# Optimization experiments

Hardware: AMD Instinct MI355X
Metric: run time of the kernel (lower is better)

## Reference

```python
import jax, jax.numpy as jnp
import numpy as np

B, H, W, C = 2, 128, 128, 96
L = H * W
NUM_HEADS = 6
D_STATE = 16
DT_RANK = 6  # ceil(96/16)
D_CONV = 4
MLP_HIDDEN = 4 * C


def _layernorm(x, g, b, eps=1e-5):
    m = x.mean(-1, keepdims=True)
    v = x.var(-1, keepdims=True)
    return (x - m) * jax.lax.rsqrt(v + eps) * g + b


def _dwconv2d(x, w, b):
    # x: [B,C,H,W], w: [C,1,3,3] depthwise, padding=1 (torch 'same' for k=3)
    y = jax.lax.conv_general_dilated(x, w, (1, 1), [(1, 1), (1, 1)],
                                     dimension_numbers=('NCHW', 'OIHW', 'NCHW'),
                                     feature_group_count=x.shape[1])
    return y + b[None, :, None, None]


def _dwconv1d(x, w):
    # x: [B,C,L], w: [C,1,4]; torch padding='same' for even k=4 pads (1,2); bias is None (conv_bias//2 == 0)
    return jax.lax.conv_general_dilated(x, w, (1,), [(1, 2)],
                                        dimension_numbers=('NCH', 'OIH', 'NCH'),
                                        feature_group_count=x.shape[1])


def _rope(x):
    # x: [b, H, W, c]; 2D axial rotary embedding, k_max = c//4 per axis
    b, h, w, c = x.shape
    k_max = c // 4
    theta = 1.0 / (10000.0 ** (jnp.arange(k_max, dtype=jnp.float32) / k_max))
    ang_h = jnp.broadcast_to(jnp.arange(h, dtype=jnp.float32)[:, None, None] * theta, (h, w, k_max))
    ang_w = jnp.broadcast_to(jnp.arange(w, dtype=jnp.float32)[None, :, None] * theta, (h, w, k_max))
    angles = jnp.concatenate([ang_h, ang_w], -1)  # [h,w,c//2]
    cos, sin = jnp.cos(angles), jnp.sin(angles)
    xr, xi = x[..., 0::2], x[..., 1::2]  # consecutive pairs -> complex
    out_r = xr * cos - xi * sin
    out_i = xr * sin + xi * cos
    return jnp.stack([out_r, out_i], -1).reshape(x.shape)


def _linear_attention(x, qk_w, qk_b, lepe_w, lepe_b):
    # x: [b, n, c]
    b, n, c = x.shape
    hd = c // NUM_HEADS
    qk = x @ qk_w + qk_b  # [b,n,2c]
    q = jax.nn.elu(qk[..., :c]) + 1.0
    k = jax.nn.elu(qk[..., c:]) + 1.0
    v = x
    q_r = _rope(q.reshape(b, H, W, c)).reshape(b, n, NUM_HEADS, hd).transpose(0, 2, 1, 3)
    k_r = _rope(k.reshape(b, H, W, c)).reshape(b, n, NUM_HEADS, hd).transpose(0, 2, 1, 3)
    qh = q.reshape(b, n, NUM_HEADS, hd).transpose(0, 2, 1, 3)
    kh = k.reshape(b, n, NUM_HEADS, hd).transpose(0, 2, 1, 3)
    vh = v.reshape(b, n, NUM_HEADS, hd).transpose(0, 2, 1, 3)
    kmean = kh.mean(axis=2, keepdims=True)  # [b,h,1,hd]
    zden = 1.0 / (jnp.einsum('bhnd,bhmd->bhnm', qh, kmean) + 1e-6)  # [b,h,n,1]
    scale = n ** (-0.5)
    kv = jnp.einsum('bhnd,bhne->bhde', k_r * scale, vh * scale)  # [b,h,hd,hd]
    out = jnp.einsum('bhnd,bhde->bhne', q_r, kv) * zden
    out = out.transpose(0, 2, 1, 3).reshape(b, n, c)
    v2d = v.reshape(b, H, W, c).transpose(0, 3, 1, 2)
    lepe = _dwconv2d(v2d, lepe_w, lepe_b).transpose(0, 2, 3, 1).reshape(b, n, c)
    return out + lepe


def _selective_scan(u, delta, A, Bm, Cm, Dv):
    # u, delta: [b,d,l]; A: [d,n]; Bm, Cm: [b,n,l]; Dv: [d]
    dA = jnp.exp(jnp.einsum('bdl,dn->lbdn', delta, A))
    dBu = jnp.einsum('bdl,bnl,bdl->lbdn', delta, Bm, u)
    Ct = jnp.moveaxis(Cm, -1, 0)  # [l,b,n]

    def step(hcar, inp):
        dA_t, dBu_t, C_t = inp
        hcar = dA_t * hcar + dBu_t  # [b,d,n]
        y_t = jnp.einsum('bdn,bn->bd', hcar, C_t)
        return hcar, y_t

    h0 = jnp.zeros(dA.shape[1:], dtype=u.dtype)
    _, ys = jax.lax.scan(step, h0, (dA, dBu, Ct))  # ys: [l,b,d]
    y = jnp.moveaxis(ys, 0, -1)  # [b,d,l]
    return y + Dv[None, :, None] * u


def setup_inputs() -> dict:
    key = jax.random.key(0)
    ks = iter(jax.random.split(key, 40))

    def rn(shape, s=0.02):
        return jax.random.normal(next(ks), shape, jnp.float32) * s

    dt = jnp.exp(jax.random.uniform(next(ks), (C,), jnp.float32)
                 * (np.log(0.1) - np.log(0.001)) + np.log(0.001))
    dt_proj_b = dt + jnp.log(-jnp.expm1(-dt))
    return {
        'hidden_states': jax.random.normal(next(ks), (B, L, C), jnp.float32),
        'norm_in_g': jnp.ones((C,), jnp.float32),
        'norm_in_b': jnp.zeros((C,), jnp.float32),
        'in_proj_w': rn((C, 3 * C)),
        'dw_w': rn((C, 1, 3, 3)),
        'dw_b': rn((C,)),
        'qk_w': rn((C, 2 * C)),
        'qk_b': rn((2 * C,)),
        'lepe_w': rn((C, 1, 3, 3)),
        'lepe_b': rn((C,)),
        'conv_x_w': rn((C, 1, D_CONV)),
        'conv_z_w': rn((C, 1, D_CONV)),
        'x_proj_w': rn((C, DT_RANK + 2 * D_STATE)),
        'dt_proj_w': rn((DT_RANK, C), DT_RANK ** -0.5),
        'dt_proj_b': dt_proj_b,
        'A_log': jnp.log(jnp.broadcast_to(jnp.arange(1, D_STATE + 1, dtype=jnp.float32), (C, D_STATE)) + 0.0),
        'D': jnp.ones((C,), jnp.float32),
        'out_proj_w': rn((2 * C, C)),
        'proj_out_w': rn((C, C)),
        'proj_out_b': rn((C,)),
        'out_w': rn((2 * C, C)),
        'out_b': rn((C,)),
        'norm_mlp_g': jnp.ones((C,), jnp.float32),
        'norm_mlp_b': jnp.zeros((C,), jnp.float32),
        'fc1_w': rn((C, MLP_HIDDEN)),
        'fc1_b': rn((MLP_HIDDEN,)),
        'fc2_w': rn((MLP_HIDDEN, C)),
        'fc2_b': rn((C,)),
    }


def reference(hidden_states, norm_in_g, norm_in_b, in_proj_w, dw_w, dw_b, qk_w, qk_b,
              lepe_w, lepe_b, conv_x_w, conv_z_w, x_proj_w, dt_proj_w, dt_proj_b,
              A_log, D, out_proj_w, proj_out_w, proj_out_b, out_w, out_b,
              norm_mlp_g, norm_mlp_b, fc1_w, fc1_b, fc2_w, fc2_b):
    b, l, c = hidden_states.shape
    shortcut = hidden_states
    hs = _layernorm(hidden_states, norm_in_g, norm_in_b)
    xzw = jnp.transpose(hs @ in_proj_w, (0, 2, 1))  # [b,3c,l]
    x, z, w_ = jnp.split(xzw, 3, axis=1)  # each [b,c,l]
    # linear-attention branch
    lin_x = jax.nn.silu(_dwconv2d(w_.reshape(b, c, H, W), dw_w, dw_b))
    lin_x = jnp.transpose(lin_x, (0, 2, 3, 1)).reshape(b, l, c)
    lin_x = _linear_attention(lin_x, qk_w, qk_b, lepe_w, lepe_b)
    # selective-scan branch
    A = -jnp.exp(A_log)
    x = jax.nn.silu(_dwconv1d(x, conv_x_w))
    z = jax.nn.silu(_dwconv1d(z, conv_z_w))
    x_dbl = jnp.einsum('bdl,de->ble', x, x_proj_w)
    dt = x_dbl[..., :DT_RANK]
    Bm = jnp.transpose(x_dbl[..., DT_RANK:DT_RANK + D_STATE], (0, 2, 1))
    Cm = jnp.transpose(x_dbl[..., DT_RANK + D_STATE:], (0, 2, 1))
    delta = jax.nn.softplus(jnp.einsum('blr,rd->bdl', dt, dt_proj_w) + dt_proj_b[None, :, None])
    y = _selective_scan(x, delta, A, Bm, Cm, D)
    y = jnp.concatenate([y, z], axis=1)  # [b,2c,l]
    out1 = jnp.transpose(y, (0, 2, 1)) @ out_proj_w  # [b,l,c]
    z_t = jnp.transpose(z, (0, 2, 1))
    out2 = (lin_x * z_t) @ proj_out_w + proj_out_b
    out = jnp.concatenate([out1, out2], -1) @ out_w + out_b
    out = shortcut + out
    h2 = _layernorm(out, norm_mlp_g, norm_mlp_b)
    h2 = jax.nn.gelu(h2 @ fc1_w + fc1_b, approximate=False)
    return out + (h2 @ fc2_w + fc2_b)
```

## Files before the change

kernel.cpp:

```cpp
#include <hip/hip_runtime.h>
#include <hip/hip_bf16.h>
#include <math.h>

#define B_ 2
#define H_ 128
#define W_ 128
#define C_ 96
#define L_ (H_*W_)
#define BL_ (B_*L_)
#define NH_ 6
#define NPROJ_ 38
#define MLPH_ 384
#define NCH_ 256
#define CHL_ (L_/NCH_)

typedef __attribute__((ext_vector_type(8))) short bf16x8;
typedef __attribute__((ext_vector_type(4))) float f32x4;

#define MFMA16(a,b,c) __builtin_amdgcn_mfma_f32_16x16x32_bf16(a,b,c,0,0,0)

#define WOFF1 0
#define WOFF2 54
#define WOFF3 90
#define WOFF4 126
#define WOFF5 144
#define WOFF6 180
#define WOFF7 252
#define WOFF8 324
#define WFRAGS 333

__device__ __forceinline__ float siluf(float x){ return x / (1.f + __expf(-x)); }
__device__ __forceinline__ unsigned short f2bf(float x){
    __hip_bfloat16 h = __float2bfloat16(x);
    return *reinterpret_cast<unsigned short*>(&h);
}
__device__ __forceinline__ unsigned pack2(float a, float b){
    return (unsigned)f2bf(a) | ((unsigned)f2bf(b) << 16);
}
__device__ __forceinline__ float bf2f(unsigned short u){
    return __uint_as_float((unsigned)u << 16);
}

__global__ __launch_bounds__(64) void k_setup(const float* __restrict__ w1,
    const float* __restrict__ w2, const float* __restrict__ w3,
    const float* __restrict__ w4, const float* __restrict__ w5,
    const float* __restrict__ w6, const float* __restrict__ w7,
    const float* __restrict__ dww, const float* __restrict__ lw,
    const float* __restrict__ xpw, const float* __restrict__ cxw,
    const float* __restrict__ czw,
    unsigned short* __restrict__ dst, float2* __restrict__ ctab,
    float* __restrict__ wt9, float* __restrict__ lw9, float* __restrict__ kvacc,
    float* __restrict__ wxT, float* __restrict__ wzT)
{
    int m = blockIdx.y;
    int l = threadIdx.x;
    if (m < 7){
        const float* srcs[7] = {w1,w2,w3,w4,w5,w6,w7};
        const int Ks[7]   = {96,96,192,96,192,96,384};
        const int Ns[7]   = {288,192,96,96,96,384,96};
        const int offs[7] = {WOFF1,WOFF2,WOFF3,WOFF4,WOFF5,WOFF6,WOFF7};
        int f = blockIdx.x;
        int nnt = Ns[m] >> 4, nkf = Ks[m] >> 5;
        if (f >= nnt*nkf) return;
        int kf = f / nnt, nt = f - kf*nnt;
        const float* s = srcs[m];
        unsigned short* d = dst + ((size_t)(offs[m] + f)*64 + l)*8;
        int krow = kf*32 + (l>>4)*8;
        int col  = nt*16 + (l&15);
        #pragma unroll
        for (int j=0;j<8;j++) d[j] = f2bf(s[(size_t)(krow+j)*Ns[m] + col]);
    } else {
        int x = blockIdx.x;
        if (x == 0){
            for (int i=l; i<128*24; i+=64){
                int pos = i/24, p = i%24;
                float th = powf(10000.f, -(float)p/24.f);
                float sn, cs; sincosf((float)pos*th, &sn, &cs);
                ctab[i] = make_float2(cs, sn);
            }
        } else if (x == 1){
            for (int i=l; i<3264; i+=64) kvacc[i] = 0.f;
        } else if (x == 2){
            for (int i=l; i<864; i+=64){
                int c = i/9, tap = i%9;
                wt9[tap*96 + c] = dww[i];
                lw9[tap*96 + c] = lw[i];
            }
        } else if (x == 3){
            for (int f=0; f<9; f++){
                int kf=f/3, nt=f%3;
                unsigned short* d = dst + ((size_t)(WOFF8 + f)*64 + l)*8;
                int krow = kf*32 + (l>>4)*8;
                int col  = nt*16 + (l&15);
                #pragma unroll
                for (int j=0;j<8;j++){
                    float v = (col < NPROJ_) ? xpw[(size_t)(krow+j)*NPROJ_ + col] : 0.f;
                    d[j] = f2bf(v);
                }
            }
        } else if (x == 4){
            for (int i=l; i<384; i+=64){
                int j = i/96, c = i%96;
                wxT[i] = cxw[c*4 + j];
                wzT[i] = czw[c*4 + j];
            }
        }
    }
}

__global__ __launch_bounds__(256) void k_ln_inproj_m(const float* __restrict__ hs,
    const float* __restrict__ gg, const float* __restrict__ bb,
    const unsigned short* __restrict__ wbf,
    float* __restrict__ xx, float* __restrict__ zz, float* __restrict__ ww)
{
    __shared__ unsigned short A[64*128];
    int t = threadIdx.x;
    size_t row0 = (size_t)blockIdx.x * 64;
    {
        int r = t >> 2, q = t & 3;
        const float* src = hs + (row0 + r)*C_ + q*24;
        float v[24];
        float s=0.f, s2=0.f;
        #pragma unroll
        for (int i=0;i<24;i++){ float x=src[i]; v[i]=x; s+=x; s2+=x*x; }
        s += __shfl_xor(s,1); s2 += __shfl_xor(s2,1);
        s += __shfl_xor(s,2); s2 += __shfl_xor(s2,2);
        float mn = s*(1.f/C_);
        float rs = rsqrtf(s2*(1.f/C_) - mn*mn + 1e-5f);
        int base = r*128, sw = (r&7)<<3;
        #pragma unroll
        for (int i=0;i<24;i+=2){
            int c = q*24 + i;
            float a0 = (v[i]  -mn)*rs*gg[c]   + bb[c];
            float a1 = (v[i+1]-mn)*rs*gg[c+1] + bb[c+1];
            *(unsigned*)&A[base + (c ^ sw)] = pack2(a0,a1);
        }
    }
    __syncthreads();
    int w = t>>6, l = t&63, lr = l&15, lh = l>>4;
    int arow = w*16 + lr;
    int abase = arow*128, asw = (arow&7)<<3;
    bf16x8 af[3];
    #pragma unroll
    for (int kf=0;kf<3;kf++)
        af[kf] = *(const bf16x8*)&A[abase + ((kf*32 + lh*8) ^ asw)];
    #pragma unroll 2
    for (int nt=0; nt<18; nt++){
        f32x4 acc = {0.f,0.f,0.f,0.f};
        #pragma unroll
        for (int kf=0;kf<3;kf++){
            bf16x8 bf_ = *(const bf16x8*)(wbf + ((size_t)((WOFF1 + kf*18 + nt)*64 + l))*8);
            acc = MFMA16(af[kf], bf_, acc);
        }
        float* base_;
        if (nt < 6) base_ = xx; else if (nt < 12) base_ = zz; else base_ = ww;
        int col = (nt%6)*16 + lr;
        float* dst = base_ + (row0 + w*16 + lh*4)*C_ + col;
        #pragma unroll
        for (int j=0;j<4;j++) dst[(size_t)j*C_] = acc[j];
    }
}

__global__ __launch_bounds__(256) void k_dwconv2d(const float* __restrict__ wwb,
    const float* __restrict__ wt9, const float* __restrict__ dwb,
    float* __restrict__ out)
{
    int gid = blockIdx.x*256 + threadIdx.x;
    int row = gid/24, c4 = gid%24; int c = c4*4;
    int b = row >> 14;
    int ll = row & (L_-1);
    int h = ll >> 7, wq = ll & 127;
    float4 acc = {0.f,0.f,0.f,0.f};
    #pragma unroll
    for (int kh=0; kh<3; kh++){
        int hh = h + kh - 1;
        if ((unsigned)hh < 128u){
            int base_row = (b<<14) + (hh<<7);
            #pragma unroll
            for (int kw=0; kw<3; kw++){
                int wp = wq + kw - 1;
                if ((unsigned)wp < 128u){
                    float4 v = *(const float4*)&wwb[(size_t)(base_row + wp)*C_ + c];
                    float4 wt = *(const float4*)&wt9[(kh*3+kw)*96 + c];
                    acc.x += v.x*wt.x; acc.y += v.y*wt.y;
                    acc.z += v.z*wt.z; acc.w += v.w*wt.w;
                }
            }
        }
    }
    float4 bv = *(const float4*)&dwb[c];
    float4 o;
    o.x = siluf(acc.x+bv.x); o.y = siluf(acc.y+bv.y);
    o.z = siluf(acc.z+bv.z); o.w = siluf(acc.w+bv.w);
    *(float4*)&out[(size_t)row*C_ + c] = o;
}

__global__ __launch_bounds__(256) void k_conv1d_xdbl(const float* __restrict__ xxb,
    const float* __restrict__ zzb, const float* __restrict__ wxT,
    const float* __restrict__ wzT, const unsigned short* __restrict__ wbf,
    const float* __restrict__ dtw, const float* __restrict__ dtb,
    float* __restrict__ xs, float* __restrict__ zs,
    float* __restrict__ delta, float* __restrict__ BC)
{
    __shared__ unsigned short A[64*128];
    __shared__ float XD[64][8];
    __shared__ float dtws[6][96];
    int t = threadIdx.x;
    size_t row0 = (size_t)blockIdx.x * 64;
    int b = (int)(row0 >> 14);
    int l0 = (int)(row0 & 16383);
    for (int i=t; i<576; i+=256) dtws[i/96][i%96] = dtw[i];
    for (int p=t; p<64*24; p+=256){
        int r = p/24, cq = p - r*24, c = cq*4;
        int l = l0 + r;
        float ax0=0.f,ax1=0.f,ax2=0.f,ax3=0.f;
        float az0=0.f,az1=0.f,az2=0.f,az3=0.f;
        #pragma unroll
        for (int j=0;j<4;j++){
            int lq = l - 1 + j;
            if ((unsigned)lq < (unsigned)L_){
                size_t off = ((size_t)(b<<14) + lq)*C_ + c;
                float4 xv = *(const float4*)&xxb[off];
                float4 zv = *(const float4*)&zzb[off];
                float4 wx4 = *(const float4*)&wxT[j*96 + c];
                float4 wz4 = *(const float4*)&wzT[j*96 + c];
                ax0 += xv.x*wx4.x; ax1 += xv.y*wx4.y; ax2 += xv.z*wx4.z; ax3 += xv.w*wx4.w;
                az0 += zv.x*wz4.x; az1 += zv.y*wz4.y; az2 += zv.z*wz4.z; az3 += zv.w*wz4.w;
            }
        }
        ax0=siluf(ax0); ax1=siluf(ax1); ax2=siluf(ax2); ax3=siluf(ax3);
        az0=siluf(az0); az1=siluf(az1); az2=siluf(az2); az3=siluf(az3);
        float4 xo={ax0,ax1,ax2,ax3}, zo={az0,az1,az2,az3};
        *(float4*)&xs[(row0+r)*C_ + c] = xo;
        *(float4*)&zs[(row0+r)*C_ + c] = zo;
        int sw = (r&7)<<3;
        uint2 pk = { pack2(ax0,ax1), pack2(ax2,ax3) };
        *(uint2*)&A[r*128 + (c ^ sw)] = pk;
    }
    __syncthreads();
    int w=t>>6, l=t&63, lr=l&15, lh=l>>4;
    int arow = w*16+lr, asw=(arow&7)<<3;
    bf16x8 af[3];
    #pragma unroll
    for (int kf=0;kf<3;kf++)
        af[kf] = *(const bf16x8*)&A[arow*128 + ((kf*32 + lh*8) ^ asw)];
    #pragma unroll
    for (int nt=0; nt<3; nt++){
        f32x4 acc={0.f,0.f,0.f,0.f};
        #pragma unroll
        for (int kf=0;kf<3;kf++){
            bf16x8 bfr=*(const bf16x8*)(wbf + ((size_t)((WOFF8 + kf*3 + nt)*64 + l))*8);
            acc = MFMA16(af[kf], bfr, acc);
        }
        int col = nt*16 + lr;
        #pragma unroll
        for (int j=0;j<4;j++){
            int row = w*16 + lh*4 + j;
            if (col < 6) XD[row][col] = acc[j];
            else if (col < NPROJ_) BC[(row0+row)*32 + (col-6)] = acc[j];
        }
    }
    __syncthreads();
    {
        int r = t>>2, q = t&3;
        float xd0=XD[r][0], xd1=XD[r][1], xd2=XD[r][2];
        float xd3=XD[r][3], xd4=XD[r][4], xd5=XD[r][5];
        #pragma unroll
        for (int g=0; g<6; g++){
            int c = q*24 + g*4;
            float4 acc = *(const float4*)&dtb[c];
            float4 w0 = *(const float4*)&dtws[0][c];
            float4 w1 = *(const float4*)&dtws[1][c];
            float4 w2 = *(const float4*)&dtws[2][c];
            float4 w3 = *(const float4*)&dtws[3][c];
            float4 w4 = *(const float4*)&dtws[4][c];
            float4 w5 = *(const float4*)&dtws[5][c];
            acc.x += xd0*w0.x + xd1*w1.x + xd2*w2.x + xd3*w3.x + xd4*w4.x + xd5*w5.x;
            acc.y += xd0*w0.y + xd1*w1.y + xd2*w2.y + xd3*w3.y + xd4*w4.y + xd5*w5.y;
            acc.z += xd0*w0.z + xd1*w1.z + xd2*w2.z + xd3*w3.z + xd4*w4.z + xd5*w5.z;
            acc.w += xd0*w0.w + xd1*w1.w + xd2*w2.w + xd3*w3.w + xd4*w4.w + xd5*w5.w;
            float4 dl;
            dl.x = (acc.x>20.f)? acc.x : __logf(1.f+__expf(acc.x));
            dl.y = (acc.y>20.f)? acc.y : __logf(1.f+__expf(acc.y));
            dl.z = (acc.z>20.f)? acc.z : __logf(1.f+__expf(acc.z));
            dl.w = (acc.w>20.f)? acc.w : __logf(1.f+__expf(acc.w));
            *(float4*)&delta[(row0+r)*C_ + c] = dl;
        }
    }
}

__global__ __launch_bounds__(256) void k_qk_kv(const float* __restrict__ lin,
    const unsigned short* __restrict__ wbf, const float* __restrict__ qkb,
    const float2* __restrict__ ctab, float* __restrict__ qo,
    float* __restrict__ kvacc)
{
    __shared__ unsigned short A[64*128];
    __shared__ float KR[64*105];
    __shared__ float kmsum[96];
    int t = threadIdx.x;
    size_t row0 = (size_t)blockIdx.x * 64;
    int b = (int)(row0 >> 14);
    int l0 = (int)(row0 & 16383);
    for (int p = t; p < 64*48; p += 256){
        int r = p/48, c = (p - r*48)*2;
        float2 xy = *(const float2*)&lin[(row0 + r)*C_ + c];
        *(unsigned*)&A[r*128 + (c ^ ((r&7)<<3))] = pack2(xy.x, xy.y);
    }
    if (t < 96) kmsum[t] = 0.f;
    __syncthreads();
    int w=t>>6, l=t&63, lr=l&15, lh=l>>4;
    int arow = w*16+lr; int asw=(arow&7)<<3;
    bf16x8 af[3];
    #pragma unroll
    for (int kf=0;kf<3;kf++)
        af[kf] = *(const bf16x8*)&A[arow*128 + ((kf*32 + lh*8) ^ asw)];
    #pragma unroll 2
    for (int nt=0; nt<12; nt++){
        f32x4 acc={0.f,0.f,0.f,0.f};
        #pragma unroll
        for (int kf=0;kf<3;kf++){
            bf16x8 bfr=*(const bf16x8*)(wbf + ((size_t)((WOFF2 + kf*12 + nt)*64 + l))*8);
            acc = MFMA16(af[kf], bfr, acc);
        }
        int colg = nt*16 + lr;
        float bias = qkb[colg];
        float vv[4];
        #pragma unroll
        for (int j=0;j<4;j++){
            float v = acc[j] + bias;
            vv[j] = (v>0.f)? v+1.f : __expf(v);
        }
        if (nt < 6){
            float* dp = qo + (row0 + w*16 + lh*4)*C_ + colg;
            #pragma unroll
            for (int j=0;j<4;j++) dp[(size_t)j*C_] = vv[j];
        } else {
            int ck = colg - 96;
            atomicAdd(&kmsum[ck], vv[0]+vv[1]+vv[2]+vv[3]);
            float pv[4];
            #pragma unroll
            for (int j=0;j<4;j++) pv[j] = __shfl_xor(vv[j], 1);
            int p = ck >> 1;
            #pragma unroll
            for (int j=0;j<4;j++){
                int rl = l0 + w*16 + lh*4 + j;
                int hp = rl>>7, wp = rl&127;
                float2 cssn = (p<24)? ctab[hp*24+p] : ctab[wp*24+(p-24)];
                float kr = (ck&1)? (pv[j]*cssn.y + vv[j]*cssn.x)
                                 : (vv[j]*cssn.x - pv[j]*cssn.y);
                KR[(w*16+lh*4+j)*105 + ck] = kr;
            }
        }
    }
    __syncthreads();
    if (w < 2){
        #pragma unroll
        for (int hh=0; hh<3; hh++){
            int h = w*3 + hh;
            f32x4 acc = {0.f,0.f,0.f,0.f};
            #pragma unroll
            for (int kk=0; kk<2; kk++){
                union { bf16x8 v; unsigned short u[8]; } afu, bfu;
                #pragma unroll
                for (int j=0;j<8;j++){
                    int rr = kk*32 + lh*8 + j;
                    afu.u[j] = f2bf(KR[rr*105 + h*16 + lr]);
                    bfu.u[j] = A[rr*128 + ((h*16+lr) ^ ((rr&7)<<3))];
                }
                acc = MFMA16(afu.v, bfu.v, acc);
            }
            #pragma unroll
            for (int i=0;i<4;i++)
                atomicAdd(&kvacc[b*1536 + h*256 + (lh*4+i)*16 + lr], acc[i]);
        }
    }
    if (t < 96) atomicAdd(&kvacc[3072 + b*96 + t], kmsum[t]);
}

__global__ __launch_bounds__(384) void k_attnout(const float* __restrict__ qbuf,
    const float* __restrict__ vbuf, const float* __restrict__ kvacc,
    const float2* __restrict__ ctab, const float* __restrict__ lw9,
    const float* __restrict__ lb, float* __restrict__ aout)
{
    __shared__ float kvs[1536];
    __shared__ float kms[96];
    int t = threadIdx.x;
    size_t row0 = (size_t)blockIdx.x * 16;
    int b = (int)(row0 >> 14);
    const float invL = 1.f/16384.f;
    for (int i=t; i<1536; i+=384) kvs[i] = kvacc[b*1536+i]*invL;
    if (t < 96) kms[t] = kvacc[3072+b*96+t]*invL;
    __syncthreads();
    int r = t/24, c4 = t%24;
    int c = c4*4;
    int lrow = (int)(row0 & 16383) + r;
    int hp = lrow>>7, wp = lrow&127;
    size_t row = row0 + r;
    float4 q4 = *(const float4*)&qbuf[row*C_ + c];
    int p0 = c>>1, p1 = p0+1;
    float2 cs0 = (p0<24)? ctab[hp*24+p0] : ctab[wp*24+(p0-24)];
    float2 cs1 = (p1<24)? ctab[hp*24+p1] : ctab[wp*24+(p1-24)];
    float4 qr;
    qr.x = q4.x*cs0.x - q4.y*cs0.y;
    qr.y = q4.x*cs0.y + q4.y*cs0.x;
    qr.z = q4.z*cs1.x - q4.w*cs1.y;
    qr.w = q4.z*cs1.y + q4.w*cs1.x;
    int h = c4>>2, j = c4&3;
    int dbase = j*4;
    float zp = q4.x*kms[h*16+dbase]   + q4.y*kms[h*16+dbase+1]
             + q4.z*kms[h*16+dbase+2] + q4.w*kms[h*16+dbase+3];
    zp += __shfl_xor(zp,1);
    zp += __shfl_xor(zp,2);
    float zd = 1.f/(zp + 1e-6f);
    float4 o = {0.f,0.f,0.f,0.f};
    #pragma unroll
    for (int g=0; g<4; g++){
        float4 qg;
        if (g==0) qg = qr;
        else {
            qg.x=__shfl_xor(qr.x,g); qg.y=__shfl_xor(qr.y,g);
            qg.z=__shfl_xor(qr.z,g); qg.w=__shfl_xor(qr.w,g);
        }
        int db = ((j^g)<<2);
        const float* kp = &kvs[h*256 + db*16 + j*4];
        #pragma unroll
        for (int i=0;i<4;i++){
            float qi = (i==0)?qg.x:(i==1)?qg.y:(i==2)?qg.z:qg.w;
            float4 kv4 = *(const float4*)&kp[i*16];
            o.x += qi*kv4.x; o.y += qi*kv4.y;
            o.z += qi*kv4.z; o.w += qi*kv4.w;
        }
    }
    float4 acc = *(const float4*)&lb[c];
    #pragma unroll
    for (int kh=0; kh<3; kh++){
        int hh = hp + kh - 1;
        if ((unsigned)hh < 128u){
            int base_row = (b<<14) + (hh<<7);
            #pragma unroll
            for (int kw=0; kw<3; kw++){
                int wq = wp + kw - 1;
                if ((unsigned)wq < 128u){
                    float4 v = *(const float4*)&vbuf[(size_t)(base_row + wq)*C_ + c];
                    float4 wt = *(const float4*)&lw9[(kh*3+kw)*96 + c];
                    acc.x += v.x*wt.x; acc.y += v.y*wt.y;
                    acc.z += v.z*wt.z; acc.w += v.w*wt.w;
                }
            }
        }
    }
    float4 res;
    res.x = o.x*zd + acc.x; res.y = o.y*zd + acc.y;
    res.z = o.z*zd + acc.z; res.w = o.w*zd + acc.w;
    *(float4*)&aout[row*C_ + c] = res;
}

__global__ __launch_bounds__(384) void k_scan1(const float* __restrict__ delta,
    const float* __restrict__ xs, const float* __restrict__ BC,
    const float* __restrict__ A_log, float* __restrict__ Ap, float* __restrict__ Be)
{
    int t = threadIdx.x; int nq = t&3, c = t>>2;
    int blk = blockIdx.x; int b = blk>>8, ch = blk&255;
    float4 a4 = *(const float4*)&A_log[c*16 + nq*4];
    float a0=-__expf(a4.x), a1=-__expf(a4.y), a2=-__expf(a4.z), a3=-__expf(a4.w);
    float ap0=1.f,ap1=1.f,ap2=1.f,ap3=1.f;
    float be0=0.f,be1=0.f,be2=0.f,be3=0.f;
    size_t base = ((size_t)b<<14) + ch*CHL_;
    for (int i=0;i<CHL_;i++){
        size_t row = base + i;
        float dl = delta[row*C_+c];
        float u  = xs[row*C_+c];
        float du = dl*u;
        float4 bc = *(const float4*)&BC[row*32 + nq*4];
        float e0=__expf(dl*a0), e1=__expf(dl*a1), e2=__expf(dl*a2), e3=__expf(dl*a3);
        ap0*=e0; be0=be0*e0+du*bc.x;
        ap1*=e1; be1=be1*e1+du*bc.y;
        ap2*=e2; be2=be2*e2+du*bc.z;
        ap3*=e3; be3=be3*e3+du*bc.w;
    }
    size_t o = (size_t)blk*1536 + c*16 + nq*4;
    float4 apv={ap0,ap1,ap2,ap3}, bev={be0,be1,be2,be3};
    *(float4*)&Ap[o] = apv;
    *(float4*)&Be[o] = bev;
}

__global__ __launch_bounds__(384) void k_scan2a(const float* __restrict__ Ap,
    const float* __restrict__ Be, float* __restrict__ GA, float* __restrict__ GB)
{
    int t = threadIdx.x; int blk = blockIdx.x;
    int b = blk>>4, g = blk&15;
    int idx = (t>>2)*16 + (t&3)*4;
    float4 A = {1.f,1.f,1.f,1.f}, Bv = {0.f,0.f,0.f,0.f};
    for (int j=0;j<16;j++){
        size_t o = ((size_t)(b*256 + g*16 + j))*1536 + idx;
        float4 a = *(const float4*)&Ap[o];
        float4 bb = *(const float4*)&Be[o];
        Bv.x=a.x*Bv.x+bb.x; Bv.y=a.y*Bv.y+bb.y; Bv.z=a.z*Bv.z+bb.z; Bv.w=a.w*Bv.w+bb.w;
        A.x*=a.x; A.y*=a.y; A.z*=a.z; A.w*=a.w;
    }
    size_t o = (size_t)blk*1536 + idx;
    *(float4*)&GA[o] = A;
    *(float4*)&GB[o] = Bv;
}

__global__ __launch_bounds__(256) void k_scan2b(const float* __restrict__ GA,
    const float* __restrict__ GB, float* __restrict__ Gin)
{
    int t = blockIdx.x*256 + threadIdx.x;
    int b = t/1536, m = t%1536;
    float h = 0.f;
    for (int g=0; g<16; g++){
        size_t o = ((size_t)(b*16+g))*1536 + m;
        Gin[o] = h;
        h = GA[o]*h + GB[o];
    }
}

__global__ __launch_bounds__(384) void k_scan2c(const float* __restrict__ Ap,
    const float* __restrict__ Be, const float* __restrict__ Gin,
    float* __restrict__ Hin)
{
    int t = threadIdx.x; int blk = blockIdx.x;
    int b = blk>>4, g = blk&15;
    int idx = (t>>2)*16 + (t&3)*4;
    float4 h = *(const float4*)&Gin[(size_t)blk*1536 + idx];
    for (int j=0;j<16;j++){
        size_t o = ((size_t)(b*256 + g*16 + j))*1536 + idx;
        *(float4*)&Hin[o] = h;
        float4 a = *(const float4*)&Ap[o];
        float4 bb = *(const float4*)&Be[o];
        h.x=a.x*h.x+bb.x; h.y=a.y*h.y+bb.y; h.z=a.z*h.z+bb.z; h.w=a.w*h.w+bb.w;
    }
}

__global__ __launch_bounds__(384) void k_scan3(const float* __restrict__ delta,
    const float* __restrict__ xs, const float* __restrict__ BC,
    const float* __restrict__ A_log, const float* __restrict__ Dv,
    const float* __restrict__ Hin, float* __restrict__ y)
{
    int t = threadIdx.x; int nq = t&3, c = t>>2;
    int blk = blockIdx.x; int b = blk>>8, ch = blk&255;
    float4 a4 = *(const float4*)&A_log[c*16 + nq*4];
    float a0=-__expf(a4.x), a1=-__expf(a4.y), a2=-__expf(a4.z), a3=-__expf(a4.w);
    float4 h = *(const float4*)&Hin[(size_t)blk*1536 + c*16 + nq*4];
    float Dc = Dv[c];
    size_t base = ((size_t)b<<14) + ch*CHL_;
    for (int i=0;i<CHL_;i++){
        size_t row = base + i;
        float dl = delta[row*C_+c];
        float u  = xs[row*C_+c];
        float du = dl*u;
        float4 bcB = *(const float4*)&BC[row*32 + nq*4];
        float4 bcC = *(const float4*)&BC[row*32 + 16 + nq*4];
        float e0=__expf(dl*a0), e1=__expf(dl*a1), e2=__expf(dl*a2), e3=__expf(dl*a3);
        h.x=h.x*e0+du*bcB.x; h.y=h.y*e1+du*bcB.y;
        h.z=h.z*e2+du*bcB.z; h.w=h.w*e3+du*bcB.w;
        float yv = h.x*bcC.x + h.y*bcC.y + h.z*bcC.z + h.w*bcC.w;
        yv += __shfl_xor(yv,1);
        yv += __shfl_xor(yv,2);
        if (nq == 0) y[row*C_+c] = yv + Dc*u;
    }
}

__global__ __launch_bounds__(256) void k_combine_m(const float* __restrict__ y,
    const float* __restrict__ zs, const float* __restrict__ aout,
    const unsigned short* __restrict__ wbf, const float* __restrict__ pob,
    const float* __restrict__ outb, const float* __restrict__ hs,
    float* __restrict__ outr)
{
    __shared__ unsigned short Y[64*192];
    __shared__ unsigned short AZ[64*128];
    __shared__ unsigned short C2[64*192];
    int t=threadIdx.x;
    size_t row0=(size_t)blockIdx.x*64;
    for (int p=t;p<64*48;p+=256){
        int r=p/48, c=(p-r*48)*2;
        size_t g=(row0+r)*C_+c;
        float2 yv=*(const float2*)&y[g];
        float2 zv=*(const float2*)&zs[g];
        float2 av=*(const float2*)&aout[g];
        int sw=(r&7)<<3;
        *(unsigned*)&Y[r*192 + (c^sw)] = pack2(yv.x,yv.y);
        *(unsigned*)&Y[r*192 + ((96+c)^sw)] = pack2(zv.x,zv.y);
        *(unsigned*)&AZ[r*128 + (c^sw)] = pack2(av.x*zv.x, av.y*zv.y);
    }
    __syncthreads();
    int w=t>>6,l=t&63,lr=l&15,lh=l>>4;
    int arow=w*16+lr; int asw=(arow&7)<<3;
    bf16x8 af1[6], af2[3];
    #pragma unroll
    for (int kf=0;kf<6;kf++) af1[kf]=*(const bf16x8*)&Y[arow*192 + ((kf*32+lh*8)^asw)];
    #pragma unroll
    for (int kf=0;kf<3;kf++) af2[kf]=*(const bf16x8*)&AZ[arow*128 + ((kf*32+lh*8)^asw)];
    #pragma unroll 2
    for (int nt=0;nt<6;nt++){
        f32x4 a1={0.f,0.f,0.f,0.f}, a2={0.f,0.f,0.f,0.f};
        #pragma unroll
        for (int kf=0;kf<6;kf++){
            bf16x8 b=*(const bf16x8*)(wbf+((size_t)((WOFF3+kf*6+nt)*64+l))*8);
            a1=MFMA16(af1[kf],b,a1);
        }
        #pragma unroll
        for (int kf=0;kf<3;kf++){
            bf16x8 b=*(const bf16x8*)(wbf+((size_t)((WOFF4+kf*6+nt)*64+l))*8);
            a2=MFMA16(af2[kf],b,a2);
        }
        int col=nt*16+lr;
        float pb=pob[col];
        #pragma unroll
        for (int j=0;j<4;j++){
            int row=w*16+lh*4+j;
            int sw2=(row&7)<<3;
            C2[row*192 + (col^sw2)] = f2bf(a1[j]);
            C2[row*192 + ((96+col)^sw2)] = f2bf(a2[j]+pb);
        }
    }
    __syncthreads();
    bf16x8 af3[6];
    #pragma unroll
    for (int kf=0;kf<6;kf++) af3[kf]=*(const bf16x8*)&C2[arow*192 + ((kf*32+lh*8)^asw)];
    #pragma unroll 2
    for (int nt=0;nt<6;nt++){
        f32x4 acc={0.f,0.f,0.f,0.f};
        #pragma unroll
        for (int kf=0;kf<6;kf++){
            bf16x8 b=*(const bf16x8*)(wbf+((size_t)((WOFF5+kf*6+nt)*64+l))*8);
            acc=MFMA16(af3[kf],b,acc);
        }
        int col=nt*16+lr;
        float ob=outb[col];
        #pragma unroll
        for (int j=0;j<4;j++){
            size_t row=row0+w*16+lh*4+j;
            outr[row*C_+col] = acc[j] + ob + hs[row*C_+col];
        }
    }
}

__global__ __launch_bounds__(256) void k_mlp_m(float* __restrict__ outr,
    const float* __restrict__ gg, const float* __restrict__ bb,
    const unsigned short* __restrict__ wbf,
    const float* __restrict__ f1b, const float* __restrict__ f2b)
{
    __shared__ unsigned short A[64*128];
    __shared__ unsigned short HID[64*384];
    int t=threadIdx.x;
    size_t row0=(size_t)blockIdx.x*64;
    {
        int r=t>>2, q=t&3;
        const float* src = outr + (row0+r)*C_ + q*24;
        float v[24]; float s=0.f,s2=0.f;
        #pragma unroll
        for(int i=0;i<24;i++){float x=src[i];v[i]=x;s+=x;s2+=x*x;}
        s+=__shfl_xor(s,1); s2+=__shfl_xor(s2,1);
        s+=__shfl_xor(s,2); s2+=__shfl_xor(s2,2);
        float mn=s*(1.f/C_), rs=rsqrtf(s2*(1.f/C_)-mn*mn+1e-5f);
        int base=r*128, sw=(r&7)<<3;
        #pragma unroll
        for(int i=0;i<24;i+=2){
            int c=q*24+i;
            *(unsigned*)&A[base+(c^sw)] = pack2((v[i]  -mn)*rs*gg[c]  +bb[c],
                                               (v[i+1]-mn)*rs*gg[c+1]+bb[c+1]);
        }
    }
    __syncthreads();
    int w=t>>6,l=t&63,lr=l&15,lh=l>>4;
    int arow=w*16+lr, asw=(arow&7)<<3;
    {
        bf16x8 af[3];
        #pragma unroll
        for(int kf=0;kf<3;kf++) af[kf]=*(const bf16x8*)&A[arow*128+((kf*32+lh*8)^asw)];
        #pragma unroll 2
        for(int nt=0;nt<24;nt++){
            f32x4 acc={0.f,0.f,0.f,0.f};
            #pragma unroll
            for(int kf=0;kf<3;kf++){
                bf16x8 b=*(const bf16x8*)(wbf+((size_t)((WOFF6+kf*24+nt)*64+l))*8);
                acc=MFMA16(af[kf],b,acc);
            }
            int col=nt*16+lr;
            float bias=f1b[col];
            #pragma unroll
            for(int j=0;j<4;j++){
                int row=w*16+lh*4+j;
                float x=acc[j]+bias;
                float g=0.5f*x*(1.f+erff(x*0.70710678f));
                HID[row*384 + (col^((row&7)<<3))] = f2bf(g);
            }
        }
    }
    __syncthreads();
    {
        bf16x8 af2[12];
        #pragma unroll
        for(int kf=0;kf<12;kf++) af2[kf]=*(const bf16x8*)&HID[arow*384+((kf*32+lh*8)^asw)];
        #pragma unroll 2
        for(int nt=0;nt<6;nt++){
            f32x4 acc={0.f,0.f,0.f,0.f};
            #pragma unroll
            for(int kf=0;kf<12;kf++){
                bf16x8 b=*(const bf16x8*)(wbf+((size_t)((WOFF7+kf*6+nt)*64+l))*8);
                acc=MFMA16(af2[kf],b,acc);
            }
            int col=nt*16+lr;
            float bias=f2b[col];
            #pragma unroll
            for(int j=0;j<4;j++){
                size_t row=row0+w*16+lh*4+j;
                outr[row*C_+col] += acc[j]+bias;
            }
        }
    }
}

extern "C" void kernel_launch(void* const* d_in, const int* in_sizes, int n_in,
                              void* d_out, int out_size, void* d_ws, size_t ws_size,
                              hipStream_t stream)
{
    const float* hs        = (const float*)d_in[0];
    const float* norm_in_g = (const float*)d_in[1];
    const float* norm_in_b = (const float*)d_in[2];
    const float* in_proj_w = (const float*)d_in[3];
    const float* dw_w      = (const float*)d_in[4];
    const float* dw_b      = (const float*)d_in[5];
    const float* qk_w      = (const float*)d_in[6];
    const float* qk_b      = (const float*)d_in[7];
    const float* lepe_w    = (const float*)d_in[8];
    const float* lepe_b    = (const float*)d_in[9];
    const float* conv_x_w  = (const float*)d_in[10];
    const float* conv_z_w  = (const float*)d_in[11];
    const float* x_proj_w  = (const float*)d_in[12];
    const float* dt_proj_w = (const float*)d_in[13];
    const float* dt_proj_b = (const float*)d_in[14];
    const float* A_log     = (const float*)d_in[15];
    const float* Dv        = (const float*)d_in[16];
    const float* out_proj_w= (const float*)d_in[17];
    const float* proj_out_w= (const float*)d_in[18];
    const float* proj_out_b= (const float*)d_in[19];
    const float* out_w     = (const float*)d_in[20];
    const float* out_b     = (const float*)d_in[21];
    const float* norm_mlp_g= (const float*)d_in[22];
    const float* norm_mlp_b= (const float*)d_in[23];
    const float* fc1_w     = (const float*)d_in[24];
    const float* fc1_b     = (const float*)d_in[25];
    const float* fc2_w     = (const float*)d_in[26];
    const float* fc2_b     = (const float*)d_in[27];

    float* ws = (float*)d_ws;
    size_t o = 0;
    float* xx    = ws + o; o += (size_t)BL_*C_;
    float* zz    = ws + o; o += (size_t)BL_*C_;
    float* wwb   = ws + o; o += (size_t)BL_*C_;
    float* lin_x = ws + o; o += (size_t)BL_*C_;
    float* xs    = ws + o; o += (size_t)BL_*C_;
    float* zs    = ws + o; o += (size_t)BL_*C_;
    float* delta = ws + o; o += (size_t)BL_*C_;
    float* BC    = ws + o; o += (size_t)BL_*32;
    float* Ap    = ws + o; o += (size_t)B_*NCH_*1536;
    float* Be    = ws + o; o += (size_t)B_*NCH_*1536;
    float* Hin   = ws + o; o += (size_t)B_*NCH_*1536;
    float* GA    = ws + o; o += (size_t)B_*16*1536;
    float* GB    = ws + o; o += (size_t)B_*16*1536;
    float* Gin   = ws + o; o += (size_t)B_*16*1536;
    float* kvacc = ws + o; o += 3264;
    float2* ctab = (float2*)(ws + o); o += 6144;
    float* wt9   = ws + o; o += 864;
    float* lw9   = ws + o; o += 864;
    float* wxT   = ws + o; o += 384;
    float* wzT   = ws + o; o += 384;
    unsigned short* wbf = (unsigned short*)(ws + o);

    float* qbuf = xx;
    float* ybuf = zz;
    float* aout = wwb;
    float* outr = (float*)d_out;

    k_setup<<<dim3(72,8), 64, 0, stream>>>(in_proj_w, qk_w, out_proj_w, proj_out_w,
                                           out_w, fc1_w, fc2_w, dw_w, lepe_w,
                                           x_proj_w, conv_x_w, conv_z_w,
                                           wbf, ctab, wt9, lw9, kvacc, wxT, wzT);
    k_ln_inproj_m<<<BL_/64, 256, 0, stream>>>(hs, norm_in_g, norm_in_b, wbf, xx, zz, wwb);
    k_dwconv2d<<<(BL_*24)/256, 256, 0, stream>>>(wwb, wt9, dw_b, lin_x);
    k_conv1d_xdbl<<<BL_/64, 256, 0, stream>>>(xx, zz, wxT, wzT, wbf,
                                              dt_proj_w, dt_proj_b, xs, zs, delta, BC);
    k_qk_kv<<<BL_/64, 256, 0, stream>>>(lin_x, wbf, qk_b, ctab, qbuf, kvacc);
    k_attnout<<<BL_/16, 384, 0, stream>>>(qbuf, lin_x, kvacc, ctab, lw9, lepe_b, aout);
    k_scan1<<<B_*NCH_, 384, 0, stream>>>(delta, xs, BC, A_log, Ap, Be);
    k_scan2a<<<B_*16, 384, 0, stream>>>(Ap, Be, GA, GB);
    k_scan2b<<<12, 256, 0, stream>>>(GA, GB, Gin);
    k_scan2c<<<B_*16, 384, 0, stream>>>(Ap, Be, Gin, Hin);
    k_scan3<<<B_*NCH_, 384, 0, stream>>>(delta, xs, BC, A_log, Dv, Hin, ybuf);
    k_combine_m<<<BL_/64, 256, 0, stream>>>(ybuf, zs, aout, wbf, proj_out_b,
                                            out_b, hs, outr);
    k_mlp_m<<<BL_/64, 256, 0, stream>>>(outr, norm_mlp_g, norm_mlp_b, wbf,
                                        fc1_b, fc2_b);
}
```

Measured before the change: 223.8 us.

## Fuse combine with MLP, use tanh GELU, and double scan chunk count

Merges the output-combine kernel and the LayerNorm+MLP kernel into one, keeping the residual in registers and computing the LayerNorm statistics with shuffles. This removes a global write/read of the intermediate output and one launch. Replaces exact erf GELU with a tanh approximation, and doubles the number of selective-scan chunks (and group count) to raise parallelism and shorten the per-thread serial loops. The cost is a larger 64KB shared pool per block, which may lower occupancy, a small numerical deviation from the GELU approximation, and larger intermediate scan buffers.

```diff
diff --git a/kernel.cpp b/kernel.cpp
--- a/kernel.cpp
+++ b/kernel.cpp
@@ -11,8 +11,9 @@
 #define NH_ 6
 #define NPROJ_ 38
 #define MLPH_ 384
-#define NCH_ 256
+#define NCH_ 512
 #define CHL_ (L_/NCH_)
+#define NG_ 32
 
 typedef __attribute__((ext_vector_type(8))) short bf16x8;
 typedef __attribute__((ext_vector_type(4))) float f32x4;
@@ -39,6 +40,14 @@
 }
 __device__ __forceinline__ float bf2f(unsigned short u){
     return __uint_as_float((unsigned)u << 16);
+}
+__device__ __forceinline__ float gelu_fast(float x){
+    float u_ = 0.7978845608f*x*(1.f + 0.044715f*x*x);
+    float au = fabsf(u_);
+    float e = __expf(-2.f*au);
+    float th = (1.f - e)/(1.f + e);
+    th = copysignf(th, u_);
+    return 0.5f*x*(1.f + th);
 }
 
 __global__ __launch_bounds__(64) void k_setup(const float* __restrict__ w1,
@@ -460,7 +469,7 @@
     const float* __restrict__ A_log, float* __restrict__ Ap, float* __restrict__ Be)
 {
     int t = threadIdx.x; int nq = t&3, c = t>>2;
-    int blk = blockIdx.x; int b = blk>>8, ch = blk&255;
+    int blk = blockIdx.x; int b = blk>>9, ch = blk&(NCH_-1);
     float4 a4 = *(const float4*)&A_log[c*16 + nq*4];
     float a0=-__expf(a4.x), a1=-__expf(a4.y), a2=-__expf(a4.z), a3=-__expf(a4.w);
     float ap0=1.f,ap1=1.f,ap2=1.f,ap3=1.f;
@@ -488,11 +497,11 @@
     const float* __restrict__ Be, float* __restrict__ GA, float* __restrict__ GB)
 {
     int t = threadIdx.x; int blk = blockIdx.x;
-    int b = blk>>4, g = blk&15;
+    int b = blk>>5, g = blk&(NG_-1);
     int idx = (t>>2)*16 + (t&3)*4;
     float4 A = {1.f,1.f,1.f,1.f}, Bv = {0.f,0.f,0.f,0.f};
     for (int j=0;j<16;j++){
-        size_t o = ((size_t)(b*256 + g*16 + j))*1536 + idx;
+        size_t o = ((size_t)(b*NCH_ + g*16 + j))*1536 + idx;
         float4 a = *(const float4*)&Ap[o];
         float4 bb = *(const float4*)&Be[o];
         Bv.x=a.x*Bv.x+bb.x; Bv.y=a.y*Bv.y+bb.y; Bv.z=a.z*Bv.z+bb.z; Bv.w=a.w*Bv.w+bb.w;
@@ -509,8 +518,8 @@
     int t = blockIdx.x*256 + threadIdx.x;
     int b = t/1536, m = t%1536;
     float h = 0.f;
-    for (int g=0; g<16; g++){
-        size_t o = ((size_t)(b*16+g))*1536 + m;
+    for (int g=0; g<NG_; g++){
+        size_t o = ((size_t)(b*NG_+g))*1536 + m;
         Gin[o] = h;
         h = GA[o]*h + GB[o];
     }
@@ -521,11 +530,11 @@
     float* __restrict__ Hin)
 {
     int t = threadIdx.x; int blk = blockIdx.x;
-    int b = blk>>4, g = blk&15;
+    int b = blk>>5, g = blk&(NG_-1);
     int idx = (t>>2)*16 + (t&3)*4;
     float4 h = *(const float4*)&Gin[(size_t)blk*1536 + idx];
     for (int j=0;j<16;j++){
-        size_t o = ((size_t)(b*256 + g*16 + j))*1536 + idx;
+        size_t o = ((size_t)(b*NCH_ + g*16 + j))*1536 + idx;
         *(float4*)&Hin[o] = h;
         float4 a = *(const float4*)&Ap[o];
         float4 bb = *(const float4*)&Be[o];
@@ -539,7 +548,7 @@
     const float* __restrict__ Hin, float* __restrict__ y)
 {
     int t = threadIdx.x; int nq = t&3, c = t>>2;
-    int blk = blockIdx.x; int b = blk>>8, ch = blk&255;
+    int blk = blockIdx.x; int b = blk>>9, ch = blk&(NCH_-1);
     float4 a4 = *(const float4*)&A_log[c*16 + nq*4];
     float a0=-__expf(a4.x), a1=-__expf(a4.y), a2=-__expf(a4.z), a3=-__expf(a4.w);
     float4 h = *(const float4*)&Hin[(size_t)blk*1536 + c*16 + nq*4];
@@ -562,15 +571,20 @@
     }
 }
 
-__global__ __launch_bounds__(256) void k_combine_m(const float* __restrict__ y,
+__global__ __launch_bounds__(256) void k_combine_mlp(const float* __restrict__ y,
     const float* __restrict__ zs, const float* __restrict__ aout,
     const unsigned short* __restrict__ wbf, const float* __restrict__ pob,
     const float* __restrict__ outb, const float* __restrict__ hs,
+    const float* __restrict__ gg, const float* __restrict__ bb,
+    const float* __restrict__ f1b, const float* __restrict__ f2b,
     float* __restrict__ outr)
 {
-    __shared__ unsigned short Y[64*192];
-    __shared__ unsigned short AZ[64*128];
-    __shared__ unsigned short C2[64*192];
+    __shared__ __attribute__((aligned(16))) char POOL[65536];
+    unsigned short* Y  = (unsigned short*)POOL;
+    unsigned short* AZ = (unsigned short*)(POOL + 24576);
+    unsigned short* C2 = (unsigned short*)(POOL + 40960);
+    unsigned short* AT = (unsigned short*)POOL;
+    unsigned short* HID= (unsigned short*)(POOL + 16384);
     int t=threadIdx.x;
     size_t row0=(size_t)blockIdx.x*64;
     for (int p=t;p<64*48;p+=256){
@@ -619,6 +633,7 @@
     bf16x8 af3[6];
     #pragma unroll
     for (int kf=0;kf<6;kf++) af3[kf]=*(const bf16x8*)&C2[arow*192 + ((kf*32+lh*8)^asw)];
+    float outv[6][4];
     #pragma unroll 2
     for (int nt=0;nt<6;nt++){
         f32x4 acc={0.f,0.f,0.f,0.f};
@@ -632,44 +647,43 @@
         #pragma unroll
         for (int j=0;j<4;j++){
             size_t row=row0+w*16+lh*4+j;
-            outr[row*C_+col] = acc[j] + ob + hs[row*C_+col];
-        }
-    }
-}
-
-__global__ __launch_bounds__(256) void k_mlp_m(float* __restrict__ outr,
-    const float* __restrict__ gg, const float* __restrict__ bb,
-    const unsigned short* __restrict__ wbf,
-    const float* __restrict__ f1b, const float* __restrict__ f2b)
-{
-    __shared__ unsigned short A[64*128];
-    __shared__ unsigned short HID[64*384];
-    int t=threadIdx.x;
-    size_t row0=(size_t)blockIdx.x*64;
-    {
-        int r=t>>2, q=t&3;
-        const float* src = outr + (row0+r)*C_ + q*24;
-        float v[24]; float s=0.f,s2=0.f;
-        #pragma unroll
-        for(int i=0;i<24;i++){float x=src[i];v[i]=x;s+=x;s2+=x*x;}
-        s+=__shfl_xor(s,1); s2+=__shfl_xor(s2,1);
-        s+=__shfl_xor(s,2); s2+=__shfl_xor(s2,2);
-        float mn=s*(1.f/C_), rs=rsqrtf(s2*(1.f/C_)-mn*mn+1e-5f);
-        int base=r*128, sw=(r&7)<<3;
-        #pragma unroll
-        for(int i=0;i<24;i+=2){
-            int c=q*24+i;
-            *(unsigned*)&A[base+(c^sw)] = pack2((v[i]  -mn)*rs*gg[c]  +bb[c],
-                                               (v[i+1]-mn)*rs*gg[c+1]+bb[c+1]);
-        }
-    }
-    __syncthreads();
-    int w=t>>6,l=t&63,lr=l&15,lh=l>>4;
-    int arow=w*16+lr, asw=(arow&7)<<3;
+            outv[nt][j] = acc[j] + ob + hs[row*C_+col];
+        }
+    }
+    float s_[4], s2_[4];
+    #pragma unroll
+    for (int j=0;j<4;j++){
+        float s=0.f, s2=0.f;
+        #pragma unroll
+        for (int nt=0;nt<6;nt++){ float v=outv[nt][j]; s+=v; s2+=v*v; }
+        s_[j]=s; s2_[j]=s2;
+    }
+    #pragma unroll
+    for (int m=1;m<16;m<<=1){
+        #pragma unroll
+        for (int j=0;j<4;j++){
+            s_[j]  += __shfl_xor(s_[j],  m);
+            s2_[j] += __shfl_xor(s2_[j], m);
+        }
+    }
+    __syncthreads();
+    #pragma unroll
+    for (int j=0;j<4;j++){
+        float mn = s_[j]*(1.f/C_);
+        float rs = rsqrtf(s2_[j]*(1.f/C_) - mn*mn + 1e-5f);
+        int row = w*16+lh*4+j;
+        int sw2 = (row&7)<<3;
+        #pragma unroll
+        for (int nt=0;nt<6;nt++){
+            int col = nt*16+lr;
+            AT[row*128 + (col^sw2)] = f2bf((outv[nt][j]-mn)*rs*gg[col]+bb[col]);
+        }
+    }
+    __syncthreads();
     {
         bf16x8 af[3];
         #pragma unroll
-        for(int kf=0;kf<3;kf++) af[kf]=*(const bf16x8*)&A[arow*128+((kf*32+lh*8)^asw)];
+        for(int kf=0;kf<3;kf++) af[kf]=*(const bf16x8*)&AT[arow*128+((kf*32+lh*8)^asw)];
         #pragma unroll 2
         for(int nt=0;nt<24;nt++){
             f32x4 acc={0.f,0.f,0.f,0.f};
@@ -683,31 +697,29 @@
             #pragma unroll
             for(int j=0;j<4;j++){
                 int row=w*16+lh*4+j;
-                float x=acc[j]+bias;
-                float g=0.5f*x*(1.f+erff(x*0.70710678f));
-                HID[row*384 + (col^((row&7)<<3))] = f2bf(g);
+                HID[row*384 + (col^((row&7)<<3))] = f2bf(gelu_fast(acc[j]+bias));
             }
         }
     }
     __syncthreads();
     {
-        bf16x8 af2[12];
-        #pragma unroll
-        for(int kf=0;kf<12;kf++) af2[kf]=*(const bf16x8*)&HID[arow*384+((kf*32+lh*8)^asw)];
+        bf16x8 afh[12];
+        #pragma unroll
+        for(int kf=0;kf<12;kf++) afh[kf]=*(const bf16x8*)&HID[arow*384+((kf*32+lh*8)^asw)];
         #pragma unroll 2
         for(int nt=0;nt<6;nt++){
             f32x4 acc={0.f,0.f,0.f,0.f};
             #pragma unroll
             for(int kf=0;kf<12;kf++){
                 bf16x8 b=*(const bf16x8*)(wbf+((size_t)((WOFF7+kf*6+nt)*64+l))*8);
-                acc=MFMA16(af2[kf],b,acc);
+                acc=MFMA16(afh[kf],b,acc);
             }
             int col=nt*16+lr;
             float bias=f2b[col];
             #pragma unroll
             for(int j=0;j<4;j++){
                 size_t row=row0+w*16+lh*4+j;
-                outr[row*C_+col] += acc[j]+bias;
+                outr[row*C_+col] = outv[nt][j] + acc[j] + bias;
             }
         }
     }
@@ -759,9 +771,9 @@
     float* Ap    = ws + o; o += (size_t)B_*NCH_*1536;
     float* Be    = ws + o; o += (size_t)B_*NCH_*1536;
     float* Hin   = ws + o; o += (size_t)B_*NCH_*1536;
-    float* GA    = ws + o; o += (size_t)B_*16*1536;
-    float* GB    = ws + o; o += (size_t)B_*16*1536;
-    float* Gin   = ws + o; o += (size_t)B_*16*1536;
+    float* GA    = ws + o; o += (size_t)B_*NG_*1536;
+    float* GB    = ws + o; o += (size_t)B_*NG_*1536;
+    float* Gin   = ws + o; o += (size_t)B_*NG_*1536;
     float* kvacc = ws + o; o += 3264;
     float2* ctab = (float2*)(ws + o); o += 6144;
     float* wt9   = ws + o; o += 864;
@@ -786,12 +798,11 @@
     k_qk_kv<<<BL_/64, 256, 0, stream>>>(lin_x, wbf, qk_b, ctab, qbuf, kvacc);
     k_attnout<<<BL_/16, 384, 0, stream>>>(qbuf, lin_x, kvacc, ctab, lw9, lepe_b, aout);
     k_scan1<<<B_*NCH_, 384, 0, stream>>>(delta, xs, BC, A_log, Ap, Be);
-    k_scan2a<<<B_*16, 384, 0, stream>>>(Ap, Be, GA, GB);
+    k_scan2a<<<B_*NG_, 384, 0, stream>>>(Ap, Be, GA, GB);
     k_scan2b<<<12, 256, 0, stream>>>(GA, GB, Gin);
-    k_scan2c<<<B_*16, 384, 0, stream>>>(Ap, Be, Gin, Hin);
+    k_scan2c<<<B_*NG_, 384, 0, stream>>>(Ap, Be, Gin, Hin);
     k_scan3<<<B_*NCH_, 384, 0, stream>>>(delta, xs, BC, A_log, Dv, Hin, ybuf);
-    k_combine_m<<<BL_/64, 256, 0, stream>>>(ybuf, zs, aout, wbf, proj_out_b,
-                                            out_b, hs, outr);
-    k_mlp_m<<<BL_/64, 256, 0, stream>>>(outr, norm_mlp_g, norm_mlp_b, wbf,
-                                        fc1_b, fc2_b);
-}
+    k_combine_mlp<<<BL_/64, 256, 0, stream>>>(ybuf, zs, aout, wbf, proj_out_b,
+                                              out_b, hs, norm_mlp_g, norm_mlp_b,
+                                              fc1_b, fc2_b, outr);
+}
```

New measurement: 209.1 us. 6.6% less time.
